# Performance work log

Hardware: AMD Instinct MI355X
Metric: run time of the kernel (lower is better)

## Reference

```python
import jax, jax.numpy as jnp
import numpy as np

N_NODES = 50000
N_EDGES = 600000

def setup_inputs() -> dict:
    key = jax.random.key(0)
    ks = jax.random.split(key, 8)
    def w(k, shape):
        # xavier-uniform-like scale (gain for relu ~ sqrt(2))
        fan_in, fan_out = shape[1], shape[0]
        lim = np.sqrt(2.0) * np.sqrt(6.0 / (fan_in + fan_out))
        return jax.random.uniform(k, shape, jnp.float32, -lim, lim)
    return {
        "x": jax.random.normal(ks[0], (N_NODES, 128), jnp.float32),
        "W_l1": w(ks[1], (256, 128)),
        "W_r1": w(ks[2], (256, 128)),
        "W_l2": w(ks[3], (256, 256)),
        "W_r2": w(ks[4], (256, 256)),
        "W_l3": w(ks[5], (47, 256)),
        "W_r3": w(ks[6], (47, 256)),
        "edge_index": jax.random.randint(ks[7], (2, N_EDGES), 0, N_NODES, jnp.int64),
    }

def sage_conv(x, src, dst, Wl, Wr, n_nodes):
    # mean aggregation of neighbor (source) features onto targets
    msg = x[src]                                   # [E, C] gather
    deg = jax.ops.segment_sum(jnp.ones((src.shape[0],), x.dtype), dst,
                              num_segments=n_nodes)
    agg = jax.ops.segment_sum(msg, dst, num_segments=n_nodes)
    agg = agg / jnp.maximum(deg, 1.0)[:, None]
    # SAGEConv(bias=False): lin_l(aggr) + lin_r(x_root)
    return agg @ Wl.T + x @ Wr.T

def reference(x, W_l1, W_r1, W_l2, W_r2, W_l3, W_r3, edge_index):
    src, dst = edge_index[0], edge_index[1]
    n = x.shape[0]
    h = sage_conv(x, src, dst, W_l1, W_r1, n)
    h = jax.nn.relu(h)  # dropout is identity in eval mode
    h = sage_conv(h, src, dst, W_l2, W_r2, n)
    h = jax.nn.relu(h)
    h = sage_conv(h, src, dst, W_l3, W_r3, n)
    return jax.nn.log_softmax(h, axis=-1)
```

## Files before the change

### kernel.cpp

```cpp
#include <hip/hip_runtime.h>
#include <hip/hip_bf16.h>

typedef __bf16 bf16_t;
typedef __bf16 bf16x8 __attribute__((ext_vector_type(8)));
typedef __bf16 bf16x4 __attribute__((ext_vector_type(4)));
typedef float f32x4 __attribute__((ext_vector_type(4)));
typedef signed char i8x4 __attribute__((ext_vector_type(4)));
typedef signed char i8x8 __attribute__((ext_vector_type(8)));

#define NN 50000
#define NE 600000
#define POISON 0xAAAAAAAAu

__device__ __forceinline__ void gload_lds16(const void* g, void* l) {
    __builtin_amdgcn_global_load_lds(
        (const __attribute__((address_space(1))) void*)g,
        (__attribute__((address_space(3))) void*)l, 16, 0, 0);
}

__global__ void cvt_all(const float* __restrict__ x, bf16_t* __restrict__ xB,
                        signed char* __restrict__ xQ, float* __restrict__ xScale,
                        const float* __restrict__ Wl1, const float* __restrict__ Wr1,
                        const float* __restrict__ Wl2, const float* __restrict__ Wr2,
                        const float* __restrict__ Wl3, const float* __restrict__ Wr3,
                        bf16_t* __restrict__ o1l, bf16_t* __restrict__ o1r,
                        bf16_t* __restrict__ o2l, bf16_t* __restrict__ o2r,
                        bf16_t* __restrict__ o3, const int* __restrict__ ei,
                        unsigned* __restrict__ degU, unsigned short* __restrict__ rank) {
    int b = blockIdx.x;
    if (b < 2344) {
        int e = b * 256 + threadIdx.x;
        if (e < NE) {
            int d = ei[NE + e];
            int rep = b & 7;
            unsigned old = atomicAdd(&degU[(long)rep * NN + d], 1u);
            rank[e] = (unsigned short)(old - POISON);
        }
    } else if (b < 8594) {
        int hw = threadIdx.x >> 5, sub = threadIdx.x & 31;
        int row = (b - 2344) * 8 + hw;
        float4 v = *(const float4*)(x + (long)row * 128 + sub * 4);
        bf16x4 o;
        o[0] = (bf16_t)v.x; o[1] = (bf16_t)v.y; o[2] = (bf16_t)v.z; o[3] = (bf16_t)v.w;
        *(bf16x4*)(xB + (long)row * 128 + sub * 4) = o;
        float m = fmaxf(fmaxf(fabsf(v.x), fabsf(v.y)), fmaxf(fabsf(v.z), fabsf(v.w)));
#pragma unroll
        for (int o2 = 1; o2 < 32; o2 <<= 1) m = fmaxf(m, __shfl_xor(m, o2));
        float rs = m > 0.f ? 127.f / m : 0.f;
        i8x4 q;
        q[0] = (signed char)fminf(fmaxf(rintf(v.x * rs), -127.f), 127.f);
        q[1] = (signed char)fminf(fmaxf(rintf(v.y * rs), -127.f), 127.f);
        q[2] = (signed char)fminf(fmaxf(rintf(v.z * rs), -127.f), 127.f);
        q[3] = (signed char)fminf(fmaxf(rintf(v.w * rs), -127.f), 127.f);
        *(i8x4*)(xQ + (long)row * 128 + sub * 4) = q;
        if (sub == 0) xScale[row] = m * (1.f / 127.f);
    } else {
        int t = (b - 8594) * 256 + threadIdx.x;
        bf16x4 o;
        if (t < 49152) {
            const float* in; bf16_t* out; int g;
            if (t < 8192)       { in = Wl1; out = o1l; g = t; }
            else if (t < 16384) { in = Wr1; out = o1r; g = t - 8192; }
            else if (t < 32768) { in = Wl2; out = o2l; g = t - 16384; }
            else                { in = Wr2; out = o2r; g = t - 32768; }
            float4 v = ((const float4*)in)[g];
            o[0] = (bf16_t)v.x; o[1] = (bf16_t)v.y; o[2] = (bf16_t)v.z; o[3] = (bf16_t)v.w;
            ((bf16x4*)out)[g] = o;
        } else if (t < 55296) {
            int g = t - 49152;
            int row = g >> 6, c4 = (g & 63) * 4;
            const float* src = nullptr;
            int srow = 0;
            if (row < 47) { src = Wl3; srow = row; }
            else if (row >= 48 && row < 95) { src = Wr3; srow = row - 48; }
            if (src) {
                float4 v = *(const float4*)(src + srow * 256 + c4);
                o[0] = (bf16_t)v.x; o[1] = (bf16_t)v.y; o[2] = (bf16_t)v.z; o[3] = (bf16_t)v.w;
            } else {
                o[0] = o[1] = o[2] = o[3] = (bf16_t)0.f;
            }
            *(bf16x4*)(o3 + row * 256 + c4) = o;
        }
    }
}

__global__ __launch_bounds__(1024) void scan_blocks(
    const unsigned* __restrict__ degU, float* __restrict__ dinv,
    int4* __restrict__ combo, int* __restrict__ partials, int n) {
    int i = blockIdx.x * 1024 + threadIdx.x;
    unsigned c[8];
    int v = 0;
    if (i < n) {
#pragma unroll
        for (int r = 0; r < 8; r++) {
            c[r] = degU[(long)r * n + i] - POISON;
            v += (int)c[r];
        }
    } else {
#pragma unroll
        for (int r = 0; r < 8; r++) c[r] = 0;
    }
    int lane = threadIdx.x & 63;
    int w = threadIdx.x >> 6;
    int s = v;
#pragma unroll
    for (int o = 1; o < 64; o <<= 1) {
        int t = __shfl_up(s, o);
        if (lane >= o) s += t;
    }
    __shared__ int wsum[16];
    if (lane == 63) wsum[w] = s;
    __syncthreads();
    if (threadIdx.x < 16) {
        int t = wsum[threadIdx.x];
#pragma unroll
        for (int o = 1; o < 16; o <<= 1) {
            int u = __shfl_up(t, o);
            if ((int)threadIdx.x >= o) t += u;
        }
        wsum[threadIdx.x] = t;
    }
    __syncthreads();
    int incl = s + ((w > 0) ? wsum[w - 1] : 0);
    if (i < n) {
        unsigned run = c[0];
        unsigned py = run;
        run += c[1]; py |= run << 8;
        run += c[2]; py |= run << 16;
        run += c[3]; py |= run << 24;
        run += c[4];
        unsigned pz = run;
        run += c[5]; pz |= run << 8;
        run += c[6]; pz |= run << 16;
        int4 cb; cb.x = incl - v; cb.y = (int)py; cb.z = (int)pz; cb.w = 0;
        combo[i] = cb;
        dinv[i] = 1.0f / fmaxf((float)v, 1.0f);
    }
    if (threadIdx.x == 1023) partials[blockIdx.x] = incl;
}

__global__ void add_offsets(int* __restrict__ rowptr, int4* __restrict__ combo,
                            const int* __restrict__ partials, int nb, int n) {
    __shared__ int bofs[64];
    __shared__ int total_s;
    if (threadIdx.x < 64) {
        int lane = threadIdx.x;
        int v = (lane < nb) ? partials[lane] : 0;
        int s = v;
#pragma unroll
        for (int o = 1; o < 64; o <<= 1) {
            int t = __shfl_up(s, o);
            if (lane >= o) s += t;
        }
        bofs[lane] = s - v;
        if (lane == nb - 1) total_s = s;
    }
    __syncthreads();
    int i = blockIdx.x * blockDim.x + threadIdx.x;
    if (i < n) {
        int4 cb = combo[i];
        cb.x += bofs[i >> 10];
        combo[i] = cb;
        rowptr[i] = cb.x;
    }
    if (blockIdx.x == 0 && threadIdx.x == 0) rowptr[n] = total_s;
}

__device__ __forceinline__ int subofs(const int4& cb, int rep) {
    if (rep == 0) return 0;
    return (rep <= 4 ? (cb.y >> ((rep - 1) * 8)) : (cb.z >> ((rep - 5) * 8))) & 0xff;
}

__global__ void fill_csr(const int* __restrict__ ei, const unsigned short* __restrict__ rank,
                         const int4* __restrict__ combo, unsigned short* __restrict__ csr_src, int E) {
    int e = (blockIdx.x * blockDim.x + threadIdx.x) * 2;
    if (e + 1 < E) {
        int rep = (e >> 8) & 7;
        int2 d = *(const int2*)(ei + E + e);
        ushort2 r = *(const ushort2*)(rank + e);
        int2 s = *(const int2*)(ei + e);
        int4 cb0 = combo[d.x];
        int4 cb1 = combo[d.y];
        int p0 = cb0.x + subofs(cb0, rep) + r.x;
        int p1 = cb1.x + subofs(cb1, rep) + r.y;
        if ((unsigned)p0 < (unsigned)E) csr_src[p0] = (unsigned short)s.x;
        if ((unsigned)p1 < (unsigned)E) csr_src[p1] = (unsigned short)s.y;
    } else if (e < E) {
        int rep = (e >> 8) & 7;
        int4 cb = combo[ei[E + e]];
        int p = cb.x + subofs(cb, rep) + rank[e];
        if ((unsigned)p < (unsigned)E) csr_src[p] = (unsigned short)ei[e];
    }
}

__global__ void gather_agg_128(const int* __restrict__ rowptr, const unsigned short* __restrict__ csr_src,
                               const signed char* __restrict__ Xq, const float* __restrict__ xScale,
                               const float* __restrict__ dinv, bf16_t* __restrict__ out, int N) {
    int wv = blockIdx.x * (blockDim.x >> 6) + (threadIdx.x >> 6);
    int lane = threadIdx.x & 63;
    int node = wv * 2 + (lane >> 5);
    if (node >= N) return;
    int sub = lane & 31;
    int hb = lane & 32;
    int c = sub * 4;
    int s0 = rowptr[node], s1 = rowptr[node + 1];
    float acc[4] = {0.f, 0.f, 0.f, 0.f};
    for (int base = s0; base < s1; base += 32) {
        int cnt = min(32, s1 - base);
        int idx = 0; float sc = 0.f;
        if (sub < cnt) { idx = csr_src[base + sub]; sc = xScale[idx]; }
        int k = 0;
        for (; k + 2 <= cnt; k += 2) {
            int i0 = __shfl(idx, hb + k), i1 = __shfl(idx, hb + k + 1);
            float c0 = __shfl(sc, hb + k), c1 = __shfl(sc, hb + k + 1);
            i8x4 v0 = *(const i8x4*)(Xq + (long)i0 * 128 + c);
            i8x4 v1 = *(const i8x4*)(Xq + (long)i1 * 128 + c);
#pragma unroll
            for (int i = 0; i < 4; i++) acc[i] += c0 * (float)v0[i] + c1 * (float)v1[i];
        }
        if (k < cnt) {
            int i0 = __shfl(idx, hb + k);
            float c0 = __shfl(sc, hb + k);
            i8x4 v0 = *(const i8x4*)(Xq + (long)i0 * 128 + c);
#pragma unroll
            for (int i = 0; i < 4; i++) acc[i] += c0 * (float)v0[i];
        }
    }
    float di = dinv[node];
    bf16x4 o;
#pragma unroll
    for (int i = 0; i < 4; i++) o[i] = (bf16_t)(acc[i] * di);
    *(bf16x4*)(out + (long)node * 128 + c) = o;
}

__global__ void gather_agg_256(const int* __restrict__ rowptr, const unsigned short* __restrict__ csr_src,
                               const signed char* __restrict__ Hq, const float* __restrict__ hScale,
                               const float* __restrict__ dinv, bf16_t* __restrict__ out, int N) {
    int wv = blockIdx.x * (blockDim.x >> 6) + (threadIdx.x >> 6);
    int lane = threadIdx.x & 63;
    int node = wv * 2 + (lane >> 5);
    if (node >= N) return;
    int sub = lane & 31;
    int hb = lane & 32;
    int c = sub * 8;
    int half = sub >> 4;
    int s0 = rowptr[node], s1 = rowptr[node + 1];
    float acc[8] = {0.f, 0.f, 0.f, 0.f, 0.f, 0.f, 0.f, 0.f};
    for (int base = s0; base < s1; base += 32) {
        int cnt = min(32, s1 - base);
        int idx = 0; float sA = 0.f, sB = 0.f;
        if (sub < cnt) {
            idx = csr_src[base + sub];
            float2 sp = *(const float2*)(hScale + idx * 2);
            sA = sp.x; sB = sp.y;
        }
        int k = 0;
        for (; k + 2 <= cnt; k += 2) {
            int i0 = __shfl(idx, hb + k), i1 = __shfl(idx, hb + k + 1);
            float a0 = __shfl(sA, hb + k), a1 = __shfl(sA, hb + k + 1);
            float b0 = __shfl(sB, hb + k), b1 = __shfl(sB, hb + k + 1);
            float c0 = half ? b0 : a0, c1 = half ? b1 : a1;
            i8x8 v0 = *(const i8x8*)(Hq + (long)i0 * 256 + c);
            i8x8 v1 = *(const i8x8*)(Hq + (long)i1 * 256 + c);
#pragma unroll
            for (int i = 0; i < 8; i++) acc[i] += c0 * (float)v0[i] + c1 * (float)v1[i];
        }
        if (k < cnt) {
            int i0 = __shfl(idx, hb + k);
            float a0 = __shfl(sA, hb + k), b0 = __shfl(sB, hb + k);
            float c0 = half ? b0 : a0;
            i8x8 v0 = *(const i8x8*)(Hq + (long)i0 * 256 + c);
#pragma unroll
            for (int i = 0; i < 8; i++) acc[i] += c0 * (float)v0[i];
        }
    }
    float di = dinv[node];
    bf16x8 o;
#pragma unroll
    for (int i = 0; i < 8; i++) o[i] = (bf16_t)(acc[i] * di);
    *(bf16x8*)(out + (long)node * 256 + c) = o;
}

template <int KTOT, bool DUAL, bool RELU, bool QUANT>
__global__ __launch_bounds__(256) void gemm_lds(
    const bf16_t* __restrict__ A1, const bf16_t* __restrict__ A2,
    const bf16_t* __restrict__ W1, const bf16_t* __restrict__ W2,
    bf16_t* __restrict__ Out, int N, int NOUT,
    signed char* __restrict__ Hq, float* __restrict__ hScale) {
    __shared__ bf16_t As[128 * 64];
    __shared__ bf16_t Bs[128 * 64];
    __shared__ float sMax[2][2][64];
    int tid = threadIdx.x;
    int w = tid >> 6, lane = tid & 63;
    int wr = w >> 1, wc = w & 1;
    int rowBase = blockIdx.x * 128;
    int colBase = blockIdx.y * 128;
    int m = lane & 15, q = lane >> 4;

    long aoff[4], boff[4];
    int ldsOff[4];
#pragma unroll
    for (int i = 0; i < 4; i++) {
        int c = w * 256 + i * 64 + lane;
        int r = c >> 3, s = c & 7;
        int gk = (s ^ (r & 7)) << 3;
        aoff[i] = (long)min(rowBase + r, N - 1) * KTOT + gk;
        boff[i] = (long)(colBase + r) * KTOT + gk;
        ldsOff[i] = (w * 4 + i) * 512;
    }

    f32x4 acc[4][4];
#pragma unroll
    for (int a = 0; a < 4; a++)
#pragma unroll
        for (int b = 0; b < 4; b++) acc[a][b] = (f32x4){0.f, 0.f, 0.f, 0.f};

#pragma unroll
    for (int half = 0; half < (DUAL ? 2 : 1); half++) {
        const bf16_t* A = half ? A2 : A1;
        const bf16_t* W = half ? W2 : W1;
#pragma unroll
        for (int k0 = 0; k0 < KTOT; k0 += 64) {
            __syncthreads();
#pragma unroll
            for (int i = 0; i < 4; i++) {
                gload_lds16(A + aoff[i] + k0, As + ldsOff[i]);
                gload_lds16(W + boff[i] + k0, Bs + ldsOff[i]);
            }
            __syncthreads();
#pragma unroll
            for (int ks = 0; ks < 2; ks++) {
                bf16x8 af[4], bfr[4];
#pragma unroll
                for (int rf = 0; rf < 4; rf++) {
                    int r = wr * 64 + rf * 16 + m;
                    int seg = ks * 4 + q;
                    af[rf] = *(const bf16x8*)(As + r * 64 + ((seg ^ (r & 7)) << 3));
                }
#pragma unroll
                for (int cf = 0; cf < 4; cf++) {
                    int r = wc * 64 + cf * 16 + m;
                    int seg = ks * 4 + q;
                    bfr[cf] = *(const bf16x8*)(Bs + r * 64 + ((seg ^ (r & 7)) << 3));
                }
#pragma unroll
                for (int rf = 0; rf < 4; rf++)
#pragma unroll
                    for (int cf = 0; cf < 4; cf++)
                        acc[rf][cf] = __builtin_amdgcn_mfma_f32_16x16x32_bf16(af[rf], bfr[cf], acc[rf][cf], 0, 0, 0);
            }
        }
    }

    int r0 = q * 4;
    if constexpr (QUANT) {
        float mm[4][4];
#pragma unroll
        for (int rf = 0; rf < 4; rf++)
#pragma unroll
            for (int i = 0; i < 4; i++) {
                float t = 0.f;
#pragma unroll
                for (int cf = 0; cf < 4; cf++) t = fmaxf(t, fmaxf(acc[rf][cf][i], 0.f));
                mm[rf][i] = t;
            }
#pragma unroll
        for (int o = 1; o < 16; o <<= 1)
#pragma unroll
            for (int rf = 0; rf < 4; rf++)
#pragma unroll
                for (int i = 0; i < 4; i++) mm[rf][i] = fmaxf(mm[rf][i], __shfl_xor(mm[rf][i], o));
        __syncthreads();
        if (m == 0) {
#pragma unroll
            for (int rf = 0; rf < 4; rf++)
#pragma unroll
                for (int i = 0; i < 4; i++) sMax[wr][wc][rf * 16 + q * 4 + i] = mm[rf][i];
        }
        __syncthreads();
#pragma unroll
        for (int rf = 0; rf < 4; rf++) {
#pragma unroll
            for (int i = 0; i < 4; i++) {
                int rowLocal = rf * 16 + r0 + i;
                int row = rowBase + wr * 64 + rowLocal;
                if (row >= N) continue;
                float rm = fmaxf(sMax[wr][0][rowLocal], sMax[wr][1][rowLocal]);
                float rs = rm > 0.f ? 127.f / rm : 0.f;
#pragma unroll
                for (int cf = 0; cf < 4; cf++) {
                    float v = fmaxf(acc[rf][cf][i], 0.f);
                    int col = colBase + wc * 64 + cf * 16 + m;
                    Out[(long)row * NOUT + col] = (bf16_t)v;
                    Hq[(long)row * NOUT + col] =
                        (signed char)fminf(rintf(v * rs), 127.f);
                }
                if (wc == 0 && m == 0)
                    hScale[row * 2 + blockIdx.y] = rm * (1.f / 127.f);
            }
        }
    } else {
#pragma unroll
        for (int rf = 0; rf < 4; rf++) {
#pragma unroll
            for (int i = 0; i < 4; i++) {
                int row = rowBase + wr * 64 + rf * 16 + r0 + i;
                if (row >= N) continue;
#pragma unroll
                for (int cf = 0; cf < 4; cf++) {
                    float v = acc[rf][cf][i];
                    if (RELU) v = fmaxf(v, 0.f);
                    Out[(long)row * NOUT + colBase + wc * 64 + cf * 16 + m] = (bf16_t)v;
                }
            }
        }
    }
}

__global__ __launch_bounds__(512, 4) void gemm2_l3(
    const bf16_t* __restrict__ A1, const bf16_t* __restrict__ A2,
    const bf16_t* __restrict__ W1, const bf16_t* __restrict__ W2,
    const bf16_t* __restrict__ W3,
    signed char* __restrict__ T3q, float* __restrict__ t3s,
    bf16_t* __restrict__ R3, int N) {
    const int K = 256;
    __shared__ bf16_t pool[128 * 256];
    bf16_t* As = pool;
    bf16_t* Bs = pool + 128 * 64;
    bf16_t* H2s = pool;
    int tid = threadIdx.x;
    int w = tid >> 6, lane = tid & 63;
    int wr = w >> 2, wc = w & 3;
    int rowBase = blockIdx.x * 128;
    int m = lane & 15, q = lane >> 4;

    long aoff[2]; int aLds[2];
    long boff[4]; int bLds[4];
#pragma unroll
    for (int i = 0; i < 2; i++) {
        int c = w * 128 + i * 64 + lane;
        int r = c >> 3, s = c & 7;
        int gk = (s ^ (r & 7)) << 3;
        aoff[i] = (long)min(rowBase + r, N - 1) * K + gk;
        aLds[i] = (w * 2 + i) * 512;
    }
#pragma unroll
    for (int i = 0; i < 4; i++) {
        int c = w * 256 + i * 64 + lane;
        int r = c >> 3, s = c & 7;
        int gk = (s ^ (r & 7)) << 3;
        boff[i] = (long)r * K + gk;
        bLds[i] = (w * 4 + i) * 512;
    }

    f32x4 acc[4][4];
#pragma unroll
    for (int a = 0; a < 4; a++)
#pragma unroll
        for (int b = 0; b < 4; b++) acc[a][b] = (f32x4){0.f, 0.f, 0.f, 0.f};

#pragma unroll
    for (int half = 0; half < 2; half++) {
        const bf16_t* A = half ? A2 : A1;
        const bf16_t* W = half ? W2 : W1;
#pragma unroll
        for (int k0 = 0; k0 < K; k0 += 64) {
            __syncthreads();
#pragma unroll
            for (int i = 0; i < 2; i++) gload_lds16(A + aoff[i] + k0, As + aLds[i]);
#pragma unroll
            for (int i = 0; i < 4; i++) gload_lds16(W + boff[i] + k0, Bs + bLds[i]);
            __syncthreads();
#pragma unroll
            for (int ks = 0; ks < 2; ks++) {
                bf16x8 af[4], bfr[4];
#pragma unroll
                for (int rf = 0; rf < 4; rf++) {
                    int r = wr * 64 + rf * 16 + m;
                    int seg = ks * 4 + q;
                    af[rf] = *(const bf16x8*)(As + r * 64 + ((seg ^ (r & 7)) << 3));
                }
#pragma unroll
                for (int cf = 0; cf < 4; cf++) {
                    int r = wc * 64 + cf * 16 + m;
                    int seg = ks * 4 + q;
                    bfr[cf] = *(const bf16x8*)(Bs + r * 64 + ((seg ^ (r & 7)) << 3));
                }
#pragma unroll
                for (int rf = 0; rf < 4; rf++)
#pragma unroll
                    for (int cf = 0; cf < 4; cf++)
                        acc[rf][cf] = __builtin_amdgcn_mfma_f32_16x16x32_bf16(af[rf], bfr[cf], acc[rf][cf], 0, 0, 0);
            }
        }
    }
    __syncthreads();

    int r0 = q * 4;
#pragma unroll
    for (int rf = 0; rf < 4; rf++)
#pragma unroll
        for (int i = 0; i < 4; i++) {
            int r = wr * 64 + rf * 16 + r0 + i;
#pragma unroll
            for (int cf = 0; cf < 4; cf++) {
                int cc = wc * 64 + cf * 16 + m;
                float v = fmaxf(acc[rf][cf][i], 0.f);
                int seg = (cc >> 3) & 7;
                H2s[r * 256 + (cc & ~63) + (((seg ^ (r & 7)) << 3)) + (cc & 7)] = (bf16_t)v;
            }
        }
    __syncthreads();

    int rg = w >> 1, cg = w & 1;
    f32x4 a3[2][3];
#pragma unroll
    for (int a = 0; a < 2; a++)
#pragma unroll
        for (int b = 0; b < 3; b++) a3[a][b] = (f32x4){0.f, 0.f, 0.f, 0.f};

#pragma unroll
    for (int kk = 0; kk < K; kk += 32) {
        int kcol = kk + q * 8;
        bf16x8 av[2], bv[3];
#pragma unroll
        for (int rf = 0; rf < 2; rf++) {
            int r = rg * 32 + rf * 16 + m;
            int seg = (kcol >> 3) & 7;
            av[rf] = *(const bf16x8*)(H2s + r * 256 + (kcol & ~63) + ((seg ^ (r & 7)) << 3));
        }
#pragma unroll
        for (int cf = 0; cf < 3; cf++)
            bv[cf] = *(const bf16x8*)(W3 + (long)(cg * 48 + cf * 16 + m) * K + kcol);
#pragma unroll
        for (int rf = 0; rf < 2; rf++)
#pragma unroll
            for (int cf = 0; cf < 3; cf++)
                a3[rf][cf] = __builtin_amdgcn_mfma_f32_16x16x32_bf16(av[rf], bv[cf], a3[rf][cf], 0, 0, 0);
    }

#pragma unroll
    for (int rf = 0; rf < 2; rf++) {
#pragma unroll
        for (int i = 0; i < 4; i++) {
            int row = rowBase + rg * 32 + rf * 16 + r0 + i;
            if (cg == 0) {
                float mmx = 0.f;
#pragma unroll
                for (int cf = 0; cf < 3; cf++) mmx = fmaxf(mmx, fabsf(a3[rf][cf][i]));
#pragma unroll
                for (int o = 1; o < 16; o <<= 1) mmx = fmaxf(mmx, __shfl_xor(mmx, o));
                if (row < N) {
                    float rs = mmx > 0.f ? 127.f / mmx : 0.f;
#pragma unroll
                    for (int cf = 0; cf < 3; cf++)
                        T3q[(long)row * 64 + cf * 16 + m] =
                            (signed char)fminf(fmaxf(rintf(a3[rf][cf][i] * rs), -127.f), 127.f);
                    if (m == 0) t3s[row] = mmx * (1.f / 127.f);
                }
            } else if (row < N) {
#pragma unroll
                for (int cf = 0; cf < 3; cf++)
                    R3[(long)row * 48 + cf * 16 + m] = (bf16_t)a3[rf][cf][i];
            }
        }
    }
}

__global__ void final_fused(const int* __restrict__ rowptr, const unsigned short* __restrict__ csr_src,
                            const signed char* __restrict__ T3q, const float* __restrict__ t3s,
                            const bf16_t* __restrict__ R3, const float* __restrict__ dinv,
                            float* __restrict__ out, int N) {
    int wv = blockIdx.x * (blockDim.x >> 6) + (threadIdx.x >> 6);
    int lane = threadIdx.x & 63;
    int node = wv * 2 + (lane >> 5);
    if (node >= N) return;
    int sub = lane & 31;
    int hb = lane & 32;
    int s0 = rowptr[node], s1 = rowptr[node + 1];
    float a0 = 0.f, a1 = 0.f;
    for (int base = s0; base < s1; base += 32) {
        int cnt = min(32, s1 - base);
        int idx = 0; float sc = 0.f;
        if (sub < cnt) { idx = csr_src[base + sub]; sc = t3s[idx]; }
        int k = 0;
        for (; k + 2 <= cnt; k += 2) {
            int i0 = __shfl(idx, hb + k), i1 = __shfl(idx, hb + k + 1);
            float c0 = __shfl(sc, hb + k), c1 = __shfl(sc, hb + k + 1);
            char2 v0 = *(const char2*)(T3q + (long)i0 * 64 + sub * 2);
            char2 v1 = *(const char2*)(T3q + (long)i1 * 64 + sub * 2);
            a0 += c0 * (float)v0.x + c1 * (float)v1.x;
            a1 += c0 * (float)v0.y + c1 * (float)v1.y;
        }
        if (k < cnt) {
            int i0 = __shfl(idx, hb + k);
            float c0 = __shfl(sc, hb + k);
            char2 v0 = *(const char2*)(T3q + (long)i0 * 64 + sub * 2);
            a0 += c0 * (float)v0.x;
            a1 += c0 * (float)v0.y;
        }
    }
    float di = dinv[node];
    int col0 = sub * 2, col1 = sub * 2 + 1;
    float v0 = (col0 < 47) ? a0 * di + (float)R3[(long)node * 48 + col0] : -INFINITY;
    float v1 = (col1 < 47) ? a1 * di + (float)R3[(long)node * 48 + col1] : -INFINITY;
    float mx = fmaxf(v0, v1);
#pragma unroll
    for (int o = 16; o; o >>= 1) mx = fmaxf(mx, __shfl_xor(mx, o));
    float s = (col0 < 47 ? expf(v0 - mx) : 0.f) + (col1 < 47 ? expf(v1 - mx) : 0.f);
#pragma unroll
    for (int o = 16; o; o >>= 1) s += __shfl_xor(s, o);
    float ls = logf(s);
    if (col0 < 47) out[(long)node * 47 + col0] = v0 - mx - ls;
    if (col1 < 47) out[(long)node * 47 + col1] = v1 - mx - ls;
}

extern "C" void kernel_launch(void* const* d_in, const int* in_sizes, int n_in,
                              void* d_out, int out_size, void* d_ws, size_t ws_size,
                              hipStream_t stream) {
    const float* x   = (const float*)d_in[0];
    const float* Wl1 = (const float*)d_in[1];
    const float* Wr1 = (const float*)d_in[2];
    const float* Wl2 = (const float*)d_in[3];
    const float* Wr2 = (const float*)d_in[4];
    const float* Wl3 = (const float*)d_in[5];
    const float* Wr3 = (const float*)d_in[6];
    const int*   ei  = (const int*)d_in[7];
    float* out = (float*)d_out;
    const int N = NN, E = NE;
    const int NB = (N + 1023) / 1024;

    char* ws = (char*)d_ws;
    size_t off = 0;
    auto carve = [&](size_t bytes) { void* p = ws + off; off = (off + bytes + 255) & ~(size_t)255; return p; };
    unsigned* degU   = (unsigned*)carve((size_t)8 * N * 4);
    int*    rowptr   = (int*)carve((size_t)(N + 1) * 4);
    int4*   combo    = (int4*)carve((size_t)N * 16);
    unsigned short* rank    = (unsigned short*)carve((size_t)E * 2);
    unsigned short* csr_src = (unsigned short*)carve((size_t)E * 2);
    int*    partials = (int*)carve(64 * 4);
    float*  dinv     = (float*)carve((size_t)N * 4);
    bf16_t* aggB     = (bf16_t*)carve((size_t)N * 256 * 2);
    bf16_t* xB       = (bf16_t*)carve((size_t)N * 128 * 2);
    signed char* xQ  = (signed char*)carve((size_t)N * 128);
    float*  xScale   = (float*)carve((size_t)N * 4);
    bf16_t* H1       = (bf16_t*)carve((size_t)N * 256 * 2);
    signed char* Hq  = (signed char*)carve((size_t)N * 256);
    float*  hScale   = (float*)carve((size_t)N * 8);
    bf16_t* H2       = (bf16_t*)carve((size_t)N * 256 * 2);
    bf16_t* wb1l = (bf16_t*)carve(256 * 128 * 2);
    bf16_t* wb1r = (bf16_t*)carve(256 * 128 * 2);
    bf16_t* wb2l = (bf16_t*)carve(256 * 256 * 2);
    bf16_t* wb2r = (bf16_t*)carve(256 * 256 * 2);
    bf16_t* wb3  = (bf16_t*)carve(96 * 256 * 2);
    signed char* T3q = (signed char*)H2;
    float*       t3s = (float*)((char*)H2 + (size_t)N * 64);
    bf16_t*      R3  = (bf16_t*)((char*)H2 + (size_t)N * 64 + (size_t)N * 4);

    cvt_all<<<2344 + 6250 + 216, 256, 0, stream>>>(x, xB, xQ, xScale,
                                                   Wl1, Wr1, Wl2, Wr2, Wl3, Wr3,
                                                   wb1l, wb1r, wb2l, wb2r, wb3, ei, degU, rank);

    scan_blocks<<<NB, 1024, 0, stream>>>(degU, dinv, combo, partials, N);
    add_offsets<<<(N + 255) / 256, 256, 0, stream>>>(rowptr, combo, partials, NB, N);
    fill_csr<<<(E / 2 + 255) / 256, 256, 0, stream>>>(ei, rank, combo, csr_src, E);

    const int RT = (N + 127) / 128;

    gather_agg_128<<<(N / 2 + 3) / 4, 256, 0, stream>>>(rowptr, csr_src, xQ, xScale, dinv, aggB, N);
    gemm_lds<128, true, true, true><<<dim3(RT, 2), 256, 0, stream>>>(
        aggB, xB, wb1l, wb1r, H1, N, 256, Hq, hScale);

    gather_agg_256<<<(N / 2 + 3) / 4, 256, 0, stream>>>(rowptr, csr_src, Hq, hScale, dinv, aggB, N);
    gemm2_l3<<<RT, 512, 0, stream>>>(aggB, H1, wb2l, wb2r, wb3, T3q, t3s, R3, N);

    final_fused<<<(N / 2 + 3) / 4, 256, 0, stream>>>(rowptr, csr_src, T3q, t3s, R3, dinv, out, N);
}
```

Before: 252.9 us.

## Fuse layer-1 gather into GEMM, merge offset add into CSR fill

The layer-1 neighbor aggregation is now computed inside the GEMM kernel: each 512-thread block gathers its 128 rows straight into a swizzled LDS tile and then runs both matmuls across all 256 output columns. This removes the aggB round-trip through global memory and one kernel launch. Quantization now uses a single per-row scale instead of two half-row scales, which simplifies the layer-2 gather. The add_offsets and fill_csr kernels are merged into one kernel that applies block offsets on the fly, saving a launch and the combo rewrite. The trade-off is a serial gather phase inside the GEMM blocks, with fewer blocks (about 391) and larger LDS use, which may reduce parallelism during the gather.

Result: no change. 254.8 us (+0.7%).

```diff
diff --git a/kernel.cpp b/kernel.cpp
--- a/kernel.cpp
+++ b/kernel.cpp
@@ -139,98 +139,232 @@
     if (threadIdx.x == 1023) partials[blockIdx.x] = incl;
 }
 
-__global__ void add_offsets(int* __restrict__ rowptr, int4* __restrict__ combo,
-                            const int* __restrict__ partials, int nb, int n) {
+__device__ __forceinline__ int subofs(const int4& cb, int rep) {
+    if (rep == 0) return 0;
+    return (rep <= 4 ? (cb.y >> ((rep - 1) * 8)) : (cb.z >> ((rep - 5) * 8))) & 0xff;
+}
+
+__global__ __launch_bounds__(256) void fill_fin(
+    const int* __restrict__ ei, const unsigned short* __restrict__ rank,
+    const int4* __restrict__ combo, const int* __restrict__ partials,
+    unsigned short* __restrict__ csr_src, int* __restrict__ rowptr,
+    int nb, int n, int E) {
     __shared__ int bofs[64];
     __shared__ int total_s;
     if (threadIdx.x < 64) {
-        int lane = threadIdx.x;
-        int v = (lane < nb) ? partials[lane] : 0;
+        int l = threadIdx.x;
+        int v = (l < nb) ? partials[l] : 0;
         int s = v;
 #pragma unroll
         for (int o = 1; o < 64; o <<= 1) {
             int t = __shfl_up(s, o);
-            if (lane >= o) s += t;
-        }
-        bofs[lane] = s - v;
-        if (lane == nb - 1) total_s = s;
+            if (l >= o) s += t;
+        }
+        bofs[l] = s - v;
+        if (l == nb - 1) total_s = s;
     }
     __syncthreads();
-    int i = blockIdx.x * blockDim.x + threadIdx.x;
-    if (i < n) {
-        int4 cb = combo[i];
-        cb.x += bofs[i >> 10];
-        combo[i] = cb;
-        rowptr[i] = cb.x;
-    }
-    if (blockIdx.x == 0 && threadIdx.x == 0) rowptr[n] = total_s;
-}
-
-__device__ __forceinline__ int subofs(const int4& cb, int rep) {
-    if (rep == 0) return 0;
-    return (rep <= 4 ? (cb.y >> ((rep - 1) * 8)) : (cb.z >> ((rep - 5) * 8))) & 0xff;
-}
-
-__global__ void fill_csr(const int* __restrict__ ei, const unsigned short* __restrict__ rank,
-                         const int4* __restrict__ combo, unsigned short* __restrict__ csr_src, int E) {
-    int e = (blockIdx.x * blockDim.x + threadIdx.x) * 2;
-    if (e + 1 < E) {
-        int rep = (e >> 8) & 7;
-        int2 d = *(const int2*)(ei + E + e);
-        ushort2 r = *(const ushort2*)(rank + e);
-        int2 s = *(const int2*)(ei + e);
-        int4 cb0 = combo[d.x];
-        int4 cb1 = combo[d.y];
-        int p0 = cb0.x + subofs(cb0, rep) + r.x;
-        int p1 = cb1.x + subofs(cb1, rep) + r.y;
-        if ((unsigned)p0 < (unsigned)E) csr_src[p0] = (unsigned short)s.x;
-        if ((unsigned)p1 < (unsigned)E) csr_src[p1] = (unsigned short)s.y;
-    } else if (e < E) {
-        int rep = (e >> 8) & 7;
-        int4 cb = combo[ei[E + e]];
-        int p = cb.x + subofs(cb, rep) + rank[e];
-        if ((unsigned)p < (unsigned)E) csr_src[p] = (unsigned short)ei[e];
-    }
-}
-
-__global__ void gather_agg_128(const int* __restrict__ rowptr, const unsigned short* __restrict__ csr_src,
-                               const signed char* __restrict__ Xq, const float* __restrict__ xScale,
-                               const float* __restrict__ dinv, bf16_t* __restrict__ out, int N) {
-    int wv = blockIdx.x * (blockDim.x >> 6) + (threadIdx.x >> 6);
-    int lane = threadIdx.x & 63;
-    int node = wv * 2 + (lane >> 5);
-    if (node >= N) return;
-    int sub = lane & 31;
-    int hb = lane & 32;
-    int c = sub * 4;
-    int s0 = rowptr[node], s1 = rowptr[node + 1];
-    float acc[4] = {0.f, 0.f, 0.f, 0.f};
-    for (int base = s0; base < s1; base += 32) {
-        int cnt = min(32, s1 - base);
-        int idx = 0; float sc = 0.f;
-        if (sub < cnt) { idx = csr_src[base + sub]; sc = xScale[idx]; }
-        int k = 0;
-        for (; k + 2 <= cnt; k += 2) {
-            int i0 = __shfl(idx, hb + k), i1 = __shfl(idx, hb + k + 1);
-            float c0 = __shfl(sc, hb + k), c1 = __shfl(sc, hb + k + 1);
-            i8x4 v0 = *(const i8x4*)(Xq + (long)i0 * 128 + c);
-            i8x4 v1 = *(const i8x4*)(Xq + (long)i1 * 128 + c);
-#pragma unroll
-            for (int i = 0; i < 4; i++) acc[i] += c0 * (float)v0[i] + c1 * (float)v1[i];
-        }
-        if (k < cnt) {
-            int i0 = __shfl(idx, hb + k);
-            float c0 = __shfl(sc, hb + k);
-            i8x4 v0 = *(const i8x4*)(Xq + (long)i0 * 128 + c);
-#pragma unroll
-            for (int i = 0; i < 4; i++) acc[i] += c0 * (float)v0[i];
-        }
-    }
-    float di = dinv[node];
-    bf16x4 o;
-#pragma unroll
-    for (int i = 0; i < 4; i++) o[i] = (bf16_t)(acc[i] * di);
-    *(bf16x4*)(out + (long)node * 128 + c) = o;
+    int b = blockIdx.x;
+    if (b < 1172) {
+        int e = (b * 256 + threadIdx.x) * 2;
+        if (e + 1 < E) {
+            int rep = (e >> 8) & 7;
+            int2 d = *(const int2*)(ei + E + e);
+            ushort2 r = *(const ushort2*)(rank + e);
+            int2 s = *(const int2*)(ei + e);
+            int4 cb0 = combo[d.x];
+            int4 cb1 = combo[d.y];
+            int p0 = cb0.x + bofs[d.x >> 10] + subofs(cb0, rep) + r.x;
+            int p1 = cb1.x + bofs[d.y >> 10] + subofs(cb1, rep) + r.y;
+            if ((unsigned)p0 < (unsigned)E) csr_src[p0] = (unsigned short)s.x;
+            if ((unsigned)p1 < (unsigned)E) csr_src[p1] = (unsigned short)s.y;
+        } else if (e < E) {
+            int rep = (e >> 8) & 7;
+            int d = ei[E + e];
+            int4 cb = combo[d];
+            int p = cb.x + bofs[d >> 10] + subofs(cb, rep) + rank[e];
+            if ((unsigned)p < (unsigned)E) csr_src[p] = (unsigned short)ei[e];
+        }
+    } else {
+        int i = (b - 1172) * 256 + threadIdx.x;
+        if (i < n) rowptr[i] = combo[i].x + bofs[i >> 10];
+        if (b == 1172 && threadIdx.x == 0) rowptr[n] = total_s;
+    }
+}
+
+__global__ __launch_bounds__(512, 4) void gemm1_fused(
+    const int* __restrict__ rowptr, const unsigned short* __restrict__ csr_src,
+    const signed char* __restrict__ Xq, const float* __restrict__ xScale,
+    const float* __restrict__ dinv, const bf16_t* __restrict__ xB,
+    const bf16_t* __restrict__ Wl1, const bf16_t* __restrict__ Wr1,
+    bf16_t* __restrict__ H1, signed char* __restrict__ Hq,
+    float* __restrict__ hScale, int N) {
+    __shared__ bf16_t pool[128 * 128 + 128 * 64 + 256 * 64];
+    bf16_t* As = pool;
+    bf16_t* A2s = pool + 128 * 128;
+    bf16_t* Bs = pool + 128 * 128 + 128 * 64;
+    float* sMax = (float*)A2s;
+    int tid = threadIdx.x;
+    int w = tid >> 6, lane = tid & 63;
+    int rowBase = blockIdx.x * 128;
+    int m = lane & 15, q = lane >> 4;
+
+    {
+        int hw = tid >> 5;
+        int sub = lane & 31;
+        int hb = lane & 32;
+        int c = sub * 4;
+        int seg = (c >> 3) & 7;
+        int cpos = (c & ~63) + (c & 7);
+#pragma unroll 1
+        for (int nn = 0; nn < 8; nn++) {
+            int rloc = hw * 8 + nn;
+            int node = rowBase + rloc;
+            float acc[4] = {0.f, 0.f, 0.f, 0.f};
+            if (node < N) {
+                int s0 = rowptr[node], s1 = rowptr[node + 1];
+                for (int base = s0; base < s1; base += 32) {
+                    int cnt = min(32, s1 - base);
+                    int idx = 0; float sc = 0.f;
+                    if (sub < cnt) { idx = csr_src[base + sub]; sc = xScale[idx]; }
+                    int k = 0;
+                    for (; k + 2 <= cnt; k += 2) {
+                        int i0 = __shfl(idx, hb + k), i1 = __shfl(idx, hb + k + 1);
+                        float c0 = __shfl(sc, hb + k), c1 = __shfl(sc, hb + k + 1);
+                        i8x4 v0 = *(const i8x4*)(Xq + (long)i0 * 128 + c);
+                        i8x4 v1 = *(const i8x4*)(Xq + (long)i1 * 128 + c);
+#pragma unroll
+                        for (int i = 0; i < 4; i++) acc[i] += c0 * (float)v0[i] + c1 * (float)v1[i];
+                    }
+                    if (k < cnt) {
+                        int i0 = __shfl(idx, hb + k);
+                        float c0 = __shfl(sc, hb + k);
+                        i8x4 v0 = *(const i8x4*)(Xq + (long)i0 * 128 + c);
+#pragma unroll
+                        for (int i = 0; i < 4; i++) acc[i] += c0 * (float)v0[i];
+                    }
+                }
+                float di = dinv[node];
+#pragma unroll
+                for (int i = 0; i < 4; i++) acc[i] *= di;
+            }
+            bf16x4 o;
+#pragma unroll
+            for (int i = 0; i < 4; i++) o[i] = (bf16_t)acc[i];
+            *(bf16x4*)(As + rloc * 128 + cpos + ((seg ^ (rloc & 7)) << 3)) = o;
+        }
+    }
+
+    int wr = w >> 2, wc = w & 3;
+    int aoff[2], aLds[2];
+    int boff[4], bLds[4];
+#pragma unroll
+    for (int i = 0; i < 2; i++) {
+        int c = (w * 2 + i) * 64 + lane;
+        int r = c >> 3, s = c & 7;
+        int gk = (s ^ (r & 7)) << 3;
+        aoff[i] = min(rowBase + r, N - 1) * 128 + gk;
+        aLds[i] = (w * 2 + i) * 512;
+    }
+#pragma unroll
+    for (int i = 0; i < 4; i++) {
+        int c = (w * 4 + i) * 64 + lane;
+        int r = c >> 3, s = c & 7;
+        int gk = (s ^ (r & 7)) << 3;
+        boff[i] = r * 128 + gk;
+        bLds[i] = (w * 4 + i) * 512;
+    }
+
+    f32x4 acc[4][4];
+#pragma unroll
+    for (int a = 0; a < 4; a++)
+#pragma unroll
+        for (int b = 0; b < 4; b++) acc[a][b] = (f32x4){0.f, 0.f, 0.f, 0.f};
+
+#pragma unroll
+    for (int half = 0; half < 2; half++) {
+        const bf16_t* W = half ? Wr1 : Wl1;
+#pragma unroll
+        for (int k0 = 0; k0 < 128; k0 += 64) {
+            __syncthreads();
+            if (half) {
+#pragma unroll
+                for (int i = 0; i < 2; i++) gload_lds16(xB + aoff[i] + k0, A2s + aLds[i]);
+            }
+#pragma unroll
+            for (int i = 0; i < 4; i++) gload_lds16(W + boff[i] + k0, Bs + bLds[i]);
+            __syncthreads();
+#pragma unroll
+            for (int ks = 0; ks < 2; ks++) {
+                bf16x8 af[4], bfr[4];
+#pragma unroll
+                for (int rf = 0; rf < 4; rf++) {
+                    int r = wr * 64 + rf * 16 + m;
+                    int seg = ks * 4 + q;
+                    af[rf] = half
+                        ? *(const bf16x8*)(A2s + r * 64 + ((seg ^ (r & 7)) << 3))
+                        : *(const bf16x8*)(As + r * 128 + k0 + ((seg ^ (r & 7)) << 3));
+                }
+#pragma unroll
+                for (int cf = 0; cf < 4; cf++) {
+                    int r = wc * 64 + cf * 16 + m;
+                    int seg = ks * 4 + q;
+                    bfr[cf] = *(const bf16x8*)(Bs + r * 64 + ((seg ^ (r & 7)) << 3));
+                }
+#pragma unroll
+                for (int rf = 0; rf < 4; rf++)
+#pragma unroll
+                    for (int cf = 0; cf < 4; cf++)
+                        acc[rf][cf] = __builtin_amdgcn_mfma_f32_16x16x32_bf16(af[rf], bfr[cf], acc[rf][cf], 0, 0, 0);
+            }
+        }
+    }
+
+    int r0 = q * 4;
+    float mm[4][4];
+#pragma unroll
+    for (int rf = 0; rf < 4; rf++)
+#pragma unroll
+        for (int i = 0; i < 4; i++) {
+            float t = 0.f;
+#pragma unroll
+            for (int cf = 0; cf < 4; cf++) t = fmaxf(t, fmaxf(acc[rf][cf][i], 0.f));
+            mm[rf][i] = t;
+        }
+#pragma unroll
+    for (int o = 1; o < 16; o <<= 1)
+#pragma unroll
+        for (int rf = 0; rf < 4; rf++)
+#pragma unroll
+            for (int i = 0; i < 4; i++) mm[rf][i] = fmaxf(mm[rf][i], __shfl_xor(mm[rf][i], o));
+    __syncthreads();
+    if (m == 0) {
+#pragma unroll
+        for (int rf = 0; rf < 4; rf++)
+#pragma unroll
+            for (int i = 0; i < 4; i++) sMax[(wr * 4 + wc) * 64 + rf * 16 + q * 4 + i] = mm[rf][i];
+    }
+    __syncthreads();
+#pragma unroll
+    for (int rf = 0; rf < 4; rf++) {
+#pragma unroll
+        for (int i = 0; i < 4; i++) {
+            int rowLocal = rf * 16 + r0 + i;
+            int row = rowBase + wr * 64 + rowLocal;
+            if (row >= N) continue;
+            float rm = fmaxf(fmaxf(sMax[(wr * 4 + 0) * 64 + rowLocal], sMax[(wr * 4 + 1) * 64 + rowLocal]),
+                             fmaxf(sMax[(wr * 4 + 2) * 64 + rowLocal], sMax[(wr * 4 + 3) * 64 + rowLocal]));
+            float rs = rm > 0.f ? 127.f / rm : 0.f;
+#pragma unroll
+            for (int cf = 0; cf < 4; cf++) {
+                float v = fmaxf(acc[rf][cf][i], 0.f);
+                int col = wc * 64 + cf * 16 + m;
+                H1[(long)row * 256 + col] = (bf16_t)v;
+                Hq[(long)row * 256 + col] = (signed char)fminf(rintf(v * rs), 127.f);
+            }
+            if (wc == 0 && m == 0) hScale[row] = rm * (1.f / 127.f);
+        }
+    }
 }
 
 __global__ void gather_agg_256(const int* __restrict__ rowptr, const unsigned short* __restrict__ csr_src,
@@ -243,23 +377,16 @@
     int sub = lane & 31;
     int hb = lane & 32;
     int c = sub * 8;
-    int half = sub >> 4;
     int s0 = rowptr[node], s1 = rowptr[node + 1];
     float acc[8] = {0.f, 0.f, 0.f, 0.f, 0.f, 0.f, 0.f, 0.f};
     for (int base = s0; base < s1; base += 32) {
         int cnt = min(32, s1 - base);
-        int idx = 0; float sA = 0.f, sB = 0.f;
-        if (sub < cnt) {
-            idx = csr_src[base + sub];
-            float2 sp = *(const float2*)(hScale + idx * 2);
-            sA = sp.x; sB = sp.y;
-        }
+        int idx = 0; float sc = 0.f;
+        if (sub < cnt) { idx = csr_src[base + sub]; sc = hScale[idx]; }
         int k = 0;
         for (; k + 2 <= cnt; k += 2) {
             int i0 = __shfl(idx, hb + k), i1 = __shfl(idx, hb + k + 1);
-            float a0 = __shfl(sA, hb + k), a1 = __shfl(sA, hb + k + 1);
-            float b0 = __shfl(sB, hb + k), b1 = __shfl(sB, hb + k + 1);
-            float c0 = half ? b0 : a0, c1 = half ? b1 : a1;
+            float c0 = __shfl(sc, hb + k), c1 = __shfl(sc, hb + k + 1);
             i8x8 v0 = *(const i8x8*)(Hq + (long)i0 * 256 + c);
             i8x8 v1 = *(const i8x8*)(Hq + (long)i1 * 256 + c);
 #pragma unroll
@@ -267,8 +394,7 @@
         }
         if (k < cnt) {
             int i0 = __shfl(idx, hb + k);
-            float a0 = __shfl(sA, hb + k), b0 = __shfl(sB, hb + k);
-            float c0 = half ? b0 : a0;
+            float c0 = __shfl(sc, hb + k);
             i8x8 v0 = *(const i8x8*)(Hq + (long)i0 * 256 + c);
 #pragma unroll
             for (int i = 0; i < 8; i++) acc[i] += c0 * (float)v0[i];
@@ -279,142 +405,6 @@
 #pragma unroll
     for (int i = 0; i < 8; i++) o[i] = (bf16_t)(acc[i] * di);
     *(bf16x8*)(out + (long)node * 256 + c) = o;
-}
-
-template <int KTOT, bool DUAL, bool RELU, bool QUANT>
-__global__ __launch_bounds__(256) void gemm_lds(
-    const bf16_t* __restrict__ A1, const bf16_t* __restrict__ A2,
-    const bf16_t* __restrict__ W1, const bf16_t* __restrict__ W2,
-    bf16_t* __restrict__ Out, int N, int NOUT,
-    signed char* __restrict__ Hq, float* __restrict__ hScale) {
-    __shared__ bf16_t As[128 * 64];
-    __shared__ bf16_t Bs[128 * 64];
-    __shared__ float sMax[2][2][64];
-    int tid = threadIdx.x;
-    int w = tid >> 6, lane = tid & 63;
-    int wr = w >> 1, wc = w & 1;
-    int rowBase = blockIdx.x * 128;
-    int colBase = blockIdx.y * 128;
-    int m = lane & 15, q = lane >> 4;
-
-    long aoff[4], boff[4];
-    int ldsOff[4];
-#pragma unroll
-    for (int i = 0; i < 4; i++) {
-        int c = w * 256 + i * 64 + lane;
-        int r = c >> 3, s = c & 7;
-        int gk = (s ^ (r & 7)) << 3;
-        aoff[i] = (long)min(rowBase + r, N - 1) * KTOT + gk;
-        boff[i] = (long)(colBase + r) * KTOT + gk;
-        ldsOff[i] = (w * 4 + i) * 512;
-    }
-
-    f32x4 acc[4][4];
-#pragma unroll
-    for (int a = 0; a < 4; a++)
-#pragma unroll
-        for (int b = 0; b < 4; b++) acc[a][b] = (f32x4){0.f, 0.f, 0.f, 0.f};
-
-#pragma unroll
-    for (int half = 0; half < (DUAL ? 2 : 1); half++) {
-        const bf16_t* A = half ? A2 : A1;
-        const bf16_t* W = half ? W2 : W1;
-#pragma unroll
-        for (int k0 = 0; k0 < KTOT; k0 += 64) {
-            __syncthreads();
-#pragma unroll
-            for (int i = 0; i < 4; i++) {
-                gload_lds16(A + aoff[i] + k0, As + ldsOff[i]);
-                gload_lds16(W + boff[i] + k0, Bs + ldsOff[i]);
-            }
-            __syncthreads();
-#pragma unroll
-            for (int ks = 0; ks < 2; ks++) {
-                bf16x8 af[4], bfr[4];
-#pragma unroll
-                for (int rf = 0; rf < 4; rf++) {
-                    int r = wr * 64 + rf * 16 + m;
-                    int seg = ks * 4 + q;
-                    af[rf] = *(const bf16x8*)(As + r * 64 + ((seg ^ (r & 7)) << 3));
-                }
-#pragma unroll
-                for (int cf = 0; cf < 4; cf++) {
-                    int r = wc * 64 + cf * 16 + m;
-                    int seg = ks * 4 + q;
-                    bfr[cf] = *(const bf16x8*)(Bs + r * 64 + ((seg ^ (r & 7)) << 3));
-                }
-#pragma unroll
-                for (int rf = 0; rf < 4; rf++)
-#pragma unroll
-                    for (int cf = 0; cf < 4; cf++)
-                        acc[rf][cf] = __builtin_amdgcn_mfma_f32_16x16x32_bf16(af[rf], bfr[cf], acc[rf][cf], 0, 0, 0);
-            }
-        }
-    }
-
-    int r0 = q * 4;
-    if constexpr (QUANT) {
-        float mm[4][4];
-#pragma unroll
-        for (int rf = 0; rf < 4; rf++)
-#pragma unroll
-            for (int i = 0; i < 4; i++) {
-                float t = 0.f;
-#pragma unroll
-                for (int cf = 0; cf < 4; cf++) t = fmaxf(t, fmaxf(acc[rf][cf][i], 0.f));
-                mm[rf][i] = t;
-            }
-#pragma unroll
-        for (int o = 1; o < 16; o <<= 1)
-#pragma unroll
-            for (int rf = 0; rf < 4; rf++)
-#pragma unroll
-                for (int i = 0; i < 4; i++) mm[rf][i] = fmaxf(mm[rf][i], __shfl_xor(mm[rf][i], o));
-        __syncthreads();
-        if (m == 0) {
-#pragma unroll
-            for (int rf = 0; rf < 4; rf++)
-#pragma unroll
-                for (int i = 0; i < 4; i++) sMax[wr][wc][rf * 16 + q * 4 + i] = mm[rf][i];
-        }
-        __syncthreads();
-#pragma unroll
-        for (int rf = 0; rf < 4; rf++) {
-#pragma unroll
-            for (int i = 0; i < 4; i++) {
-                int rowLocal = rf * 16 + r0 + i;
-                int row = rowBase + wr * 64 + rowLocal;
-                if (row >= N) continue;
-                float rm = fmaxf(sMax[wr][0][rowLocal], sMax[wr][1][rowLocal]);
-                float rs = rm > 0.f ? 127.f / rm : 0.f;
-#pragma unroll
-                for (int cf = 0; cf < 4; cf++) {
-                    float v = fmaxf(acc[rf][cf][i], 0.f);
-                    int col = colBase + wc * 64 + cf * 16 + m;
-                    Out[(long)row * NOUT + col] = (bf16_t)v;
-                    Hq[(long)row * NOUT + col] =
-                        (signed char)fminf(rintf(v * rs), 127.f);
-                }
-                if (wc == 0 && m == 0)
-                    hScale[row * 2 + blockIdx.y] = rm * (1.f / 127.f);
-            }
-        }
-    } else {
-#pragma unroll
-        for (int rf = 0; rf < 4; rf++) {
-#pragma unroll
-            for (int i = 0; i < 4; i++) {
-                int row = rowBase + wr * 64 + rf * 16 + r0 + i;
-                if (row >= N) continue;
-#pragma unroll
-                for (int cf = 0; cf < 4; cf++) {
-                    float v = acc[rf][cf][i];
-                    if (RELU) v = fmaxf(v, 0.f);
-                    Out[(long)row * NOUT + colBase + wc * 64 + cf * 16 + m] = (bf16_t)v;
-                }
-            }
-        }
-    }
 }
 
 __global__ __launch_bounds__(512, 4) void gemm2_l3(
@@ -646,7 +636,7 @@
     float*  xScale   = (float*)carve((size_t)N * 4);
     bf16_t* H1       = (bf16_t*)carve((size_t)N * 256 * 2);
     signed char* Hq  = (signed char*)carve((size_t)N * 256);
-    float*  hScale   = (float*)carve((size_t)N * 8);
+    float*  hScale   = (float*)carve((size_t)N * 4);
     bf16_t* H2       = (bf16_t*)carve((size_t)N * 256 * 2);
     bf16_t* wb1l = (bf16_t*)carve(256 * 128 * 2);
     bf16_t* wb1r = (bf16_t*)carve(256 * 128 * 2);
@@ -662,14 +652,12 @@
                                                    wb1l, wb1r, wb2l, wb2r, wb3, ei, degU, rank);
 
     scan_blocks<<<NB, 1024, 0, stream>>>(degU, dinv, combo, partials, N);
-    add_offsets<<<(N + 255) / 256, 256, 0, stream>>>(rowptr, combo, partials, NB, N);
-    fill_csr<<<(E / 2 + 255) / 256, 256, 0, stream>>>(ei, rank, combo, csr_src, E);
+    fill_fin<<<1172 + 196, 256, 0, stream>>>(ei, rank, combo, partials, csr_src, rowptr, NB, N, E);
 
     const int RT = (N + 127) / 128;
 
-    gather_agg_128<<<(N / 2 + 3) / 4, 256, 0, stream>>>(rowptr, csr_src, xQ, xScale, dinv, aggB, N);
-    gemm_lds<128, true, true, true><<<dim3(RT, 2), 256, 0, stream>>>(
-        aggB, xB, wb1l, wb1r, H1, N, 256, Hq, hScale);
+    gemm1_fused<<<RT, 512, 0, stream>>>(rowptr, csr_src, xQ, xScale, dinv, xB,
+                                        wb1l, wb1r, H1, Hq, hScale, N);
 
     gather_agg_256<<<(N / 2 + 3) / 4, 256, 0, stream>>>(rowptr, csr_src, Hq, hScale, dinv, aggB, N);
     gemm2_l3<<<RT, 512, 0, stream>>>(aggB, H1, wb2l, wb2r, wb3, T3q, t3s, R3, N);
```
